# Kernel optimization log

Measured on AMD Instinct MI355X. Metric: run time of the kernel, lower is better.

Reference implementation:

```python
import jax, jax.numpy as jnp
import numpy as np

CH = 64
HEADS = 4
HD = CH // HEADS          # 16
BLOCK = 8
HALO = 1
NEIGH = BLOCK + 2 * HALO  # 10
SR = 2
HDH = HD // 2             # 8


def conv1x1(x, w, b=None):
    y = jnp.einsum('oc,bchw->bohw', w, x)
    return y if b is None else y + b[None, :, None, None]


def dw3x3(x, w, pad_mode):
    # depthwise 3x3 conv, padding=1 with given pad mode
    xp = jnp.pad(x, ((0, 0), (0, 0), (1, 1), (1, 1)), mode=pad_mode)
    return jax.lax.conv_general_dilated(
        xp, w, (1, 1), 'VALID',
        dimension_numbers=('NCHW', 'OIHW', 'NCHW'),
        feature_group_count=x.shape[1])


def maxpool2(x):
    return jax.lax.reduce_window(x, -jnp.inf, jax.lax.max, (1, 1, 2, 2), (1, 1, 2, 2), 'VALID')


def l2norm(x):
    return x / jnp.maximum(jnp.linalg.norm(x, axis=-1, keepdims=True), 1e-12)


def sorted_channel_indices(q):
    # correlation-based channel ordering (computed under no_grad in torch)
    B, C = q.shape[0], q.shape[1]
    f = jax.lax.stop_gradient(q.reshape(B, C, -1))
    cen = f - f.mean(axis=2, keepdims=True)
    cov = jnp.einsum('bcn,bdn->bcd', cen, cen)
    std = jnp.sqrt(jnp.diagonal(cov, axis1=1, axis2=2) + 1e-8)
    denom = jnp.maximum(std[:, :, None] * std[:, None, :], 1e-8)
    sim = (cov / denom).mean(axis=2)
    return jnp.argsort(-sim, axis=1)  # descending


def up_bilinear_ac(x, s):
    # bilinear upsample, align_corners=True (torch convention)
    def lerp_axis(t, axis):
        n_in = t.shape[axis]
        n_out = n_in * s
        c = jnp.arange(n_out, dtype=t.dtype) * ((n_in - 1.0) / (n_out - 1.0))
        lo = jnp.clip(jnp.floor(c).astype(jnp.int32), 0, n_in - 2)
        w = c - lo.astype(t.dtype)
        shape = [1] * t.ndim
        shape[axis] = n_out
        w = w.reshape(shape)
        return jnp.take(t, lo, axis=axis) * (1 - w) + jnp.take(t, lo + 1, axis=axis) * w
    return lerp_axis(lerp_axis(x, 2), 3)


def _forward(x, qkv_w, lce_w, gate_w, gate_b, temp, rel_h_emb, rel_w_emb,
             down_w, down_b, up_w, up_b, gating_w, gating_b, proj_w, lp_w, lp_b):
    x_in = maxpool2(x)                         # sr=2 sampler
    B, C, H, W = x_in.shape                    # H,W divisible by BLOCK -> no pad branch
    hb, wb = H // BLOCK, W // BLOCK
    BL = B * hb * wb

    qkv = dw3x3(conv1x1(x_in, qkv_w), lce_w, 'constant')   # qkv_conv + lce
    q, k, v = jnp.split(qkv, 3, axis=1)

    idx = sorted_channel_indices(q)
    gidx = idx[:, :, None, None]
    q_s = jnp.take_along_axis(q, gidx, axis=1)
    k_s = jnp.take_along_axis(k, gidx, axis=1)
    v_s = jnp.take_along_axis(v, gidx, axis=1)

    # gating: grouped 1x1 conv, one [HD,HD] matmul per head
    qh = q_s.reshape(B, HEADS, HD, H, W)
    gate_score = jnp.einsum('goc,bgcxy->bgoxy', gate_w, qh) + gate_b[None, :, :, None, None]

    # query blocks: [BL, heads, block*block, hd]
    qi = qh.reshape(B, HEADS, HD, hb, BLOCK, wb, BLOCK)
    qi = qi.transpose(0, 3, 5, 1, 4, 6, 2).reshape(BL, HEADS, BLOCK * BLOCK, HD)

    def halo_patches(t):
        # F.unfold(kernel=NEIGH, stride=BLOCK, padding=HALO), zero pad
        tp = jnp.pad(t, ((0, 0), (0, 0), (HALO, HALO), (HALO, HALO)))
        ridx = jnp.arange(hb)[:, None] * BLOCK + jnp.arange(NEIGH)[None, :]
        cidx = jnp.arange(wb)[:, None] * BLOCK + jnp.arange(NEIGH)[None, :]
        p = tp[:, :, ridx, :][..., cidx]       # [B, C, hb, NEIGH, wb, NEIGH]
        p = p.reshape(B, HEADS, HD, hb, NEIGH, wb, NEIGH).transpose(0, 3, 5, 1, 4, 6, 2)
        return p.reshape(BL, HEADS, NEIGH, NEIGH, HD)

    ks = halo_patches(k_s)
    vi = halo_patches(v_s).reshape(BL, HEADS, NEIGH * NEIGH, HD)

    # relative positional embeddings on split key channels
    kh = ks[..., :HDH] + rel_h_emb             # [BL,heads,NEIGH,NEIGH,HDH]
    kw = ks[..., HDH:] + rel_w_emb
    ki = jnp.concatenate([kh, kw], axis=-1).reshape(BL, HEADS, NEIGH * NEIGH, HD)

    logits = jnp.einsum('bhqc,bhkc->bhqk', l2norm(qi), l2norm(ki)) * jnp.exp(temp)
    attn = jax.nn.softmax(logits, axis=-1)
    out_i = jnp.einsum('bhqk,bhkc->bhqc', attn, vi)

    out = out_i.reshape(B, hb, wb, HEADS, BLOCK, BLOCK, HD)
    out = out.transpose(0, 3, 6, 1, 4, 2, 5).reshape(B, HEADS, HD, H, W)
    out = (out * jax.nn.sigmoid(gate_score)).reshape(B, C, H, W)

    cache = q_s + k_s
    inv = jnp.argsort(idx, axis=1)[:, :, None, None]
    out = jnp.take_along_axis(out, inv, axis=1)
    cache = jnp.take_along_axis(cache, inv, axis=1)

    # Intra_CacheModulation
    mixed = out + cache
    g = jax.nn.gelu(conv1x1(mixed, gating_w, gating_b), approximate=False) * mixed
    out = out + conv1x1(conv1x1(g, down_w, down_b), up_w, up_b)

    out = conv1x1(out, proj_w)
    # LocalProp: depthwise 3x3 reflect-pad conv + bilinear x2 (align_corners=True)
    out = dw3x3(out, lp_w, 'reflect') + lp_b[None, :, None, None]
    out = up_bilinear_ac(out, SR)
    # final F.interpolate to input size is identity here (shapes already match)
    return out


def setup_inputs() -> dict:
    key = jax.random.key(0)
    ks = jax.random.split(key, 12)
    B, H, W = 4, 256, 256
    p = lambda k, shape, s=0.02: jax.random.normal(k, shape, jnp.float32) * s
    return {
        'x': jax.random.normal(ks[0], (B, CH, H, W), jnp.float32),
        'qkv_w': p(ks[1], (3 * CH, CH), 0.05),
        'lce_w': p(ks[2], (3 * CH, 1, 3, 3), 0.1),
        'gate_w': p(ks[3], (HEADS, HD, HD), 0.1),
        'gate_b': jnp.ones((HEADS, HD), jnp.float32),
        'temp': jnp.zeros((1, HEADS, 1, 1), jnp.float32),
        'rel_h_emb': p(ks[4], (1, HEADS, NEIGH, 1, HDH)),
        'rel_w_emb': p(ks[5], (1, HEADS, 1, NEIGH, HD - HDH)),
        'down_w': p(ks[6], (CH // 2, CH), 0.05),
        'down_b': jnp.zeros((CH // 2,), jnp.float32),
        'up_w': p(ks[7], (CH, CH // 2), 0.05),
        'up_b': jnp.zeros((CH,), jnp.float32),
        'gating_w': p(ks[8], (CH, CH), 0.05),
        'gating_b': jnp.zeros((CH,), jnp.float32),
        'proj_w': p(ks[9], (CH, CH), 0.05),
        'lp_w': p(ks[10], (CH, 1, 3, 3), 0.1),
        'lp_b': jnp.zeros((CH,), jnp.float32),
    }


def reference(x, qkv_w, lce_w, gate_w, gate_b, temp, rel_h_emb, rel_w_emb,
              down_w, down_b, up_w, up_b, gating_w, gating_b, proj_w, lp_w, lp_b):
    return _forward(x, qkv_w, lce_w, gate_w, gate_b, temp, rel_h_emb, rel_w_emb,
                    down_w, down_b, up_w, up_b, gating_w, gating_b, proj_w, lp_w, lp_b)
```

## Files before the change

### kernel.cpp

```cpp
#include <hip/hip_runtime.h>
#include <math.h>

#define HWP 16384

static const size_t PRE_OFF  = 0;
static const size_t QKV_OFF  = 12582912;
static const size_t WT_OFF   = QKV_OFF;
static const size_t COVP_OFF = 0;
static const size_t MEAN_OFF = 2097152;
static const size_t COVS_OFF = 2097408;
static const size_t KHAT_OFF = 0;
static const size_t VPK_OFF  = 6553600;
static const size_t OUT3_OFF = 0;
static const size_t IDX_OFF  = 12570112;
static const size_t INV_OFF  = 12570368;
static const size_t GT2_OFF  = 12570624;
static const size_t DT2_OFF  = 12574720;
static const size_t UT2_OFF  = 12576768;
static const size_t PT2_OFF  = 12578816;

__global__ __launch_bounds__(256) void k_prep_wt(
    const float* __restrict__ qkv_w, float* __restrict__ wT) {
  int i = blockIdx.x * 256 + threadIdx.x;
  int o = i >> 6, c = i & 63;
  wT[c * 192 + o] = qkv_w[i];
}

__global__ __launch_bounds__(256) void k_prep2(
    const float* __restrict__ gating_w, const float* __restrict__ down_w,
    const float* __restrict__ up_w, const float* __restrict__ proj_w,
    float* __restrict__ gT, float* __restrict__ dT,
    float* __restrict__ uT, float* __restrict__ pT) {
  int t = blockIdx.x * 256 + threadIdx.x;
  if (t < 4096) {
    int o = t >> 6, d = t & 63;
    gT[d * 64 + o] = gating_w[t];
    pT[d * 64 + o] = proj_w[t];
  }
  if (t < 2048) {
    int o = t >> 6, d = t & 63;
    dT[d * 32 + o] = down_w[t];
    int o2 = t >> 5, d2 = t & 31;
    uT[d2 * 64 + o2] = up_w[t];
  }
}

__global__ __launch_bounds__(256) void k_pool_conv(
    const float* __restrict__ x, const float* __restrict__ wT,
    float* __restrict__ pre) {
  int b = blockIdx.x >> 8;
  int pix0 = (blockIdx.x & 255) * 64;
  __shared__ float xt[64 * 64];
  int t = threadIdx.x;
  for (int i = 0; i < 16; ++i) {
    int f = i * 256 + t;
    int c = f >> 6, p = f & 63;
    int pix = pix0 + p;
    int y = pix >> 7, xx = pix & 127;
    const float* src = x + ((size_t)(b * 64 + c) * 65536) + (2 * y) * 256 + 2 * xx;
    float2 v01 = *(const float2*)src;
    float2 v23 = *(const float2*)(src + 256);
    xt[c * 64 + p] = fmaxf(fmaxf(v01.x, v01.y), fmaxf(v23.x, v23.y));
  }
  __syncthreads();
  int p = t & 63;
  int obase = __builtin_amdgcn_readfirstlane((t >> 6) * 48);
  const float* wbase = wT + obase;
  float acc[48];
#pragma unroll
  for (int j = 0; j < 48; ++j) acc[j] = 0.f;
  for (int c = 0; c < 64; ++c) {
    float xv = xt[c * 64 + p];
    const float* wc = wbase + c * 192;
#pragma unroll
    for (int j = 0; j < 48; ++j) acc[j] = fmaf(wc[j], xv, acc[j]);
  }
  float* dst = pre + ((size_t)b * 192 + obase) * HWP + pix0 + p;
#pragma unroll
  for (int j = 0; j < 48; ++j) dst[(size_t)j * HWP] = acc[j];
}

__global__ __launch_bounds__(256) void k_dw3x3_zero(
    const float* __restrict__ pre, const float* __restrict__ lce_w,
    float* __restrict__ qkv) {
  int gid = blockIdx.x * 256 + threadIdx.x;
  int c4 = gid & 31;
  int y  = (gid >> 5) & 127;
  int bc = gid >> 12;
  int ch = bc % 192;
  int x0 = c4 * 4;
  const float* base = pre + (size_t)bc * HWP;
  const float* w = lce_w + ch * 9;
  const float4 z4 = make_float4(0.f, 0.f, 0.f, 0.f);
  bool ym = y > 0, yp = y < 127;
  bool xl = x0 > 0, xr = x0 < 124;
  const float* rowm = base + (y - 1) * 128;
  const float* rowc = base + y * 128;
  const float* rowp = base + (y + 1) * 128;
  float4 vm = ym ? *(const float4*)(rowm + x0) : z4;
  float  lm = (ym && xl) ? rowm[x0 - 1] : 0.f;
  float  rm = (ym && xr) ? rowm[x0 + 4] : 0.f;
  float4 vc = *(const float4*)(rowc + x0);
  float  lc = xl ? rowc[x0 - 1] : 0.f;
  float  rc = xr ? rowc[x0 + 4] : 0.f;
  float4 vp = yp ? *(const float4*)(rowp + x0) : z4;
  float  lp = (yp && xl) ? rowp[x0 - 1] : 0.f;
  float  rp = (yp && xr) ? rowp[x0 + 4] : 0.f;
  float w0 = w[0], w1 = w[1], w2 = w[2], w3 = w[3], w4 = w[4],
        w5 = w[5], w6 = w[6], w7 = w[7], w8 = w[8];
  float4 o;
  o.x = fmaf(w8, vp.y, fmaf(w7, vp.x, fmaf(w6, lp,
        fmaf(w5, vc.y, fmaf(w4, vc.x, fmaf(w3, lc,
        fmaf(w2, vm.y, fmaf(w1, vm.x, fmaf(w0, lm, 0.f)))))))));
  o.y = fmaf(w8, vp.z, fmaf(w7, vp.y, fmaf(w6, vp.x,
        fmaf(w5, vc.z, fmaf(w4, vc.y, fmaf(w3, vc.x,
        fmaf(w2, vm.z, fmaf(w1, vm.y, fmaf(w0, vm.x, 0.f)))))))));
  o.z = fmaf(w8, vp.w, fmaf(w7, vp.z, fmaf(w6, vp.y,
        fmaf(w5, vc.w, fmaf(w4, vc.z, fmaf(w3, vc.y,
        fmaf(w2, vm.w, fmaf(w1, vm.z, fmaf(w0, vm.y, 0.f)))))))));
  o.w = fmaf(w8, rp,   fmaf(w7, vp.w, fmaf(w6, vp.z,
        fmaf(w5, rc,   fmaf(w4, vc.w, fmaf(w3, vc.z,
        fmaf(w2, rm,   fmaf(w1, vm.w, fmaf(w0, vm.z, 0.f)))))))));
  *(float4*)(qkv + (size_t)bc * HWP + y * 128 + x0) = o;
}

__global__ __launch_bounds__(256) void k_mean(
    const float* __restrict__ qkv, float* __restrict__ mean) {
  int bc = blockIdx.x;
  int b = bc >> 6, c = bc & 63;
  const float* src = qkv + ((size_t)b * 192 + c) * HWP;
  float s = 0.f;
  for (int i = threadIdx.x; i < HWP; i += 256) s += src[i];
  __shared__ float red[4];
  for (int off = 32; off > 0; off >>= 1) s += __shfl_down(s, off);
  int t = threadIdx.x;
  if ((t & 63) == 0) red[t >> 6] = s;
  __syncthreads();
  if (t == 0) mean[bc] = (red[0] + red[1] + red[2] + red[3]) * (1.f / 16384.f);
}

__global__ __launch_bounds__(256) void k_covpart(
    const float* __restrict__ qkv, const float* __restrict__ mean,
    float* __restrict__ covp) {
  int blk = blockIdx.x;
  int b = blk >> 7, chunk = blk & 127;
  int e0 = chunk * 128;
  __shared__ float qc[64 * 129];
  int t = threadIdx.x;
  for (int i = 0; i < 32; ++i) {
    int f = i * 256 + t;
    int c = f >> 7, e = f & 127;
    qc[c * 129 + e] = qkv[((size_t)b * 192 + c) * HWP + e0 + e] - mean[b * 64 + c];
  }
  __syncthreads();
  int d = t & 63;
  int crow = t >> 6;
  float acc[16];
#pragma unroll
  for (int i = 0; i < 16; ++i) acc[i] = 0.f;
  for (int e = 0; e < 128; ++e) {
    float qd = qc[d * 129 + e];
#pragma unroll
    for (int i = 0; i < 16; ++i) {
      int c = crow + 4 * i;
      acc[i] = fmaf(qc[c * 129 + e], qd, acc[i]);
    }
  }
  float* dst = covp + (size_t)blk * 4096;
#pragma unroll
  for (int i = 0; i < 16; ++i) {
    int c = crow + 4 * i;
    dst[c * 64 + d] = acc[i];
  }
}

__global__ __launch_bounds__(256) void k_covred(
    const float* __restrict__ covp, float* __restrict__ covs) {
  int blk = blockIdx.x;
  int b = blk >> 4;
  int pp = (blk & 15) * 256 + threadIdx.x;
  const float* src = covp + (size_t)b * 524288 + pp;
  float s = 0.f;
  for (int ch = 0; ch < 128; ++ch) s += src[ch * 4096];
  covs[b * 4096 + pp] = s;
}

__global__ __launch_bounds__(256) void k_simsort(
    const float* __restrict__ covs_g, int* __restrict__ idx, int* __restrict__ inv) {
  int b = blockIdx.x;
  __shared__ float covs[4096];
  __shared__ float stds[64];
  __shared__ float sims[64];
  int t = threadIdx.x;
  for (int i = 0; i < 16; ++i) covs[i * 256 + t] = covs_g[b * 4096 + i * 256 + t];
  __syncthreads();
  if (t < 64) stds[t] = sqrtf(covs[t * 64 + t] + 1e-8f);
  __syncthreads();
  if (t < 64) {
    float s = 0.f;
    float sc = stds[t];
    for (int d2 = 0; d2 < 64; ++d2) {
      float denom = fmaxf(sc * stds[d2], 1e-8f);
      s += covs[d2 * 64 + t] / denom;
    }
    sims[t] = s * (1.f / 64.f);
  }
  __syncthreads();
  if (t < 64) {
    float sv = sims[t];
    int r = 0;
    for (int d2 = 0; d2 < 64; ++d2) {
      float o = sims[d2];
      if (o > sv || (o == sv && d2 < t)) r++;
    }
    idx[b * 64 + r] = t;
    inv[b * 64 + t] = r;
  }
}

__global__ __launch_bounds__(64) void k_stage(
    const float* __restrict__ qkv, const int* __restrict__ idx,
    const float* __restrict__ rel_h, const float* __restrict__ rel_w,
    float* __restrict__ khat, float* __restrict__ vpk) {
  int bi = blockIdx.x;
  int head = bi & 3;
  int wj = (bi >> 2) & 15;
  int hi = (bi >> 6) & 15;
  int b = bi >> 10;
  int t = threadIdx.x;
  const size_t bb = (size_t)b * 192 * HWP;
  int chg[16];
#pragma unroll
  for (int ch = 0; ch < 16; ++ch) chg[ch] = idx[b * 64 + head * 16 + ch];
  for (int i = 0; i < 2; ++i) {
    int pos = i * 64 + t;
    if (pos < 100) {
      int py = pos / 10, px = pos - py * 10;
      int ky = hi * 8 + py - 1, kx = wj * 8 + px - 1;
      bool ok = (ky >= 0) && (ky < 128) && (kx >= 0) && (kx < 128);
      int sp = ky * 128 + kx;
      float kv[16];
      float s = 0.f;
#pragma unroll
      for (int ch = 0; ch < 16; ++ch) {
        float k = ok ? qkv[bb + (size_t)(64 + chg[ch]) * HWP + sp] : 0.f;
        k += (ch < 8) ? rel_h[(head * 10 + py) * 8 + ch]
                      : rel_w[(head * 10 + px) * 8 + (ch - 8)];
        kv[ch] = k;
        s += k * k;
      }
      float rn = 1.f / fmaxf(sqrtf(s), 1e-12f);
      float* kd = khat + ((size_t)bi * 100 + pos) * 16;
#pragma unroll
      for (int ch = 0; ch < 16; ++ch) kd[ch] = kv[ch] * rn;
    }
  }
  int qy = hi * 8 + (t >> 3), qx = wj * 8 + (t & 7);
  int spq = qy * 128 + qx;
  float* vd = vpk + ((size_t)(b * 4 + head) * 16384 + spq) * 16;
#pragma unroll
  for (int ch = 0; ch < 16; ++ch)
    vd[ch] = qkv[bb + (size_t)(128 + chg[ch]) * HWP + spq];
}

__global__ __launch_bounds__(128) void k_attn(
    const float* __restrict__ qkv, const int* __restrict__ idx,
    const float* __restrict__ khat, const float* __restrict__ vpk,
    const float* __restrict__ gate_w, const float* __restrict__ gate_b,
    const float* __restrict__ temp, float* __restrict__ attn_out) {
  int bi = blockIdx.x;
  int head = bi & 3;
  int wj = (bi >> 2) & 15;
  int hi = (bi >> 6) & 15;
  int b = bi >> 10;
  int tt = threadIdx.x;
  int t = tt & 63;
  int w = __builtin_amdgcn_readfirstlane(tt >> 6);
  __shared__ __align__(16) float smem[3200];
  float* kr = smem;
  float* vr = smem + 1600;
  const size_t bb = (size_t)b * 192 * HWP;
  const float* kg = khat + (size_t)bi * 1600;
  for (int f = tt; f < 400; f += 128)
    ((float4*)kr)[f] = ((const float4*)kg)[f];
  const float* vb = vpk + (size_t)(b * 4 + head) * (16384 * 16);
  for (int f = tt; f < 400; f += 128) {
    int pos = f >> 2, comp = f & 3;
    int py = pos / 10, px = pos - py * 10;
    int ky = hi * 8 + py - 1, kx = wj * 8 + px - 1;
    bool ok = (ky >= 0) && (ky < 128) && (kx >= 0) && (kx < 128);
    float4 v = make_float4(0.f, 0.f, 0.f, 0.f);
    if (ok) v = ((const float4*)(vb + (size_t)(ky * 128 + kx) * 16))[comp];
    ((float4*)vr)[f] = v;
  }
  int chg[16];
#pragma unroll
  for (int ch = 0; ch < 16; ++ch) chg[ch] = idx[b * 64 + head * 16 + ch];
  int qy = hi * 8 + (t >> 3), qx = wj * 8 + (t & 7);
  float q[16];
  float qs = 0.f;
#pragma unroll
  for (int ch = 0; ch < 16; ++ch) {
    q[ch] = qkv[bb + (size_t)chg[ch] * HWP + qy * 128 + qx];
    qs += q[ch] * q[ch];
  }
  float T = expf(temp[head]);
  float qnT = T / fmaxf(sqrtf(qs), 1e-12f);
  __syncthreads();
  float out[16];
#pragma unroll
  for (int ch = 0; ch < 16; ++ch) out[ch] = 0.f;
  float wsum = 0.f;
  for (int pyl = 0; pyl < 5; ++pyl) {
    int py = w * 5 + pyl;
    const float* kp0 = kr + py * 160;
    const float* vp0 = vr + py * 160;
    for (int px = 0; px < 10; ++px) {
      const float* kp = kp0 + px * 16;
      const float* vp = vp0 + px * 16;
      float d0 = 0.f, d1 = 0.f, d2 = 0.f, d3 = 0.f;
#pragma unroll
      for (int ch = 0; ch < 4; ++ch) {
        d0 = fmaf(q[ch], kp[ch], d0);
        d1 = fmaf(q[ch + 4], kp[ch + 4], d1);
        d2 = fmaf(q[ch + 8], kp[ch + 8], d2);
        d3 = fmaf(q[ch + 12], kp[ch + 12], d3);
      }
      float dacc = (d0 + d1) + (d2 + d3);
      float e = __expf(fmaf(dacc, qnT, -T));
      wsum += e;
#pragma unroll
      for (int ch = 0; ch < 16; ++ch)
        out[ch] = fmaf(e, vp[ch], out[ch]);
    }
  }
  __syncthreads();
  float* po = smem;
  float* pwp = smem + 2048;
  pwp[w * 64 + t] = wsum;
#pragma unroll
  for (int ch = 0; ch < 16; ++ch) po[(w * 16 + ch) * 64 + t] = out[ch];
  __syncthreads();
  float winv = 1.f / (pwp[t] + pwp[64 + t]);
  int ob = w * 8;
#pragma unroll
  for (int i = 0; i < 8; ++i) {
    int o = ob + i;
    float oc = po[o * 64 + t] + po[(16 + o) * 64 + t];
    float gsv = gate_b[head * 16 + o];
#pragma unroll
    for (int c = 0; c < 16; ++c)
      gsv = fmaf(gate_w[head * 256 + o * 16 + c], q[c], gsv);
    float sig = 1.f / (1.f + __expf(-gsv));
    attn_out[bb + (size_t)(128 + chg[o]) * HWP + qy * 128 + qx] = oc * winv * sig;
  }
}

__global__ __launch_bounds__(256) void k_post(
    const float* __restrict__ attn, const float* __restrict__ qkv,
    const float* __restrict__ gT, const float* __restrict__ gating_b,
    const float* __restrict__ dT, const float* __restrict__ down_b,
    const float* __restrict__ uT, const float* __restrict__ up_b,
    const float* __restrict__ pT, float* __restrict__ out3) {
  __shared__ float xs[64 * 64];
  int t = threadIdx.x;
  int lane = t & 63;
  int w = t >> 6;
  int p = blockIdx.x * 64 + lane;
  int b = p >> 14;
  int pix = p & 16383;
  const float* ap = attn + ((size_t)b * 192 + 128) * HWP + pix;
  const float* qp = qkv + (size_t)b * 192 * HWP + pix;
  float* op = out3 + (size_t)b * 64 * HWP + pix;
  int ob16 = __builtin_amdgcn_readfirstlane(w * 16);
  int ob8  = __builtin_amdgcn_readfirstlane(w * 8);
#pragma unroll
  for (int i = 0; i < 16; ++i) {
    int c = ob16 + i;
    xs[c * 64 + lane] = ap[(size_t)c * HWP] + qp[(size_t)c * HWP] + qp[(size_t)(64 + c) * HWP];
  }
  __syncthreads();
  {
    float acc[16];
#pragma unroll
    for (int o = 0; o < 16; ++o) acc[o] = gating_b[ob16 + o];
    for (int d = 0; d < 64; ++d) {
      float xv = xs[d * 64 + lane];
      const float* wd = gT + d * 64 + ob16;
#pragma unroll
      for (int o = 0; o < 16; ++o) acc[o] = fmaf(wd[o], xv, acc[o]);
    }
    __syncthreads();
#pragma unroll
    for (int o = 0; o < 16; ++o) {
      float a = acc[o];
      float ge = 0.5f * a * (1.f + erff(a * 0.70710678118654752f));
      xs[(ob16 + o) * 64 + lane] = ge * xs[(ob16 + o) * 64 + lane];
    }
    __syncthreads();
  }
  {
    float acc[8];
#pragma unroll
    for (int o = 0; o < 8; ++o) acc[o] = down_b[ob8 + o];
    for (int d = 0; d < 64; ++d) {
      float xv = xs[d * 64 + lane];
      const float* wd = dT + d * 32 + ob8;
#pragma unroll
      for (int o = 0; o < 8; ++o) acc[o] = fmaf(wd[o], xv, acc[o]);
    }
    __syncthreads();
#pragma unroll
    for (int o = 0; o < 8; ++o) xs[(ob8 + o) * 64 + lane] = acc[o];
    __syncthreads();
  }
  {
    float acc[16];
#pragma unroll
    for (int o = 0; o < 16; ++o) acc[o] = up_b[ob16 + o];
    for (int d = 0; d < 32; ++d) {
      float xv = xs[d * 64 + lane];
      const float* wd = uT + d * 64 + ob16;
#pragma unroll
      for (int o = 0; o < 16; ++o) acc[o] = fmaf(wd[o], xv, acc[o]);
    }
    __syncthreads();
#pragma unroll
    for (int o = 0; o < 16; ++o)
      xs[(ob16 + o) * 64 + lane] = acc[o] + ap[(size_t)(ob16 + o) * HWP];
    __syncthreads();
  }
  {
    float acc[16];
#pragma unroll
    for (int o = 0; o < 16; ++o) acc[o] = 0.f;
    for (int d = 0; d < 64; ++d) {
      float xv = xs[d * 64 + lane];
      const float* wd = pT + d * 64 + ob16;
#pragma unroll
      for (int o = 0; o < 16; ++o) acc[o] = fmaf(wd[o], xv, acc[o]);
    }
#pragma unroll
    for (int o = 0; o < 16; ++o) op[(size_t)(ob16 + o) * HWP] = acc[o];
  }
}

__global__ __launch_bounds__(256) void k_final(
    const float* __restrict__ out3, const float* __restrict__ lp_w,
    const float* __restrict__ lp_b, float* __restrict__ out) {
  int bi = blockIdx.x;
  int rt = bi & 7;
  int bc = bi >> 3;
  int ch = bc & 63;
  int r0 = rt * 16;
  __shared__ float tin[20 * 128];
  __shared__ float tdw[18 * 128];
  int t = threadIdx.x;
  const float* src = out3 + (size_t)bc * HWP;
  for (int i = 0; i < 10; ++i) {
    int f = i * 256 + t;
    int r = f >> 7, xx = f & 127;
    int ry = r0 - 2 + r;
    ry = ry < 0 ? -ry : (ry > 127 ? 254 - ry : ry);
    tin[f] = src[ry * 128 + xx];
  }
  __syncthreads();
  float w0 = lp_w[ch * 9 + 0], w1 = lp_w[ch * 9 + 1], w2 = lp_w[ch * 9 + 2];
  float w3 = lp_w[ch * 9 + 3], w4 = lp_w[ch * 9 + 4], w5 = lp_w[ch * 9 + 5];
  float w6 = lp_w[ch * 9 + 6], w7 = lp_w[ch * 9 + 7], w8 = lp_w[ch * 9 + 8];
  float bias = lp_b[ch];
  for (int i = 0; i < 9; ++i) {
    int f = i * 256 + t;
    int r = f >> 7, xx = f & 127;
    int xm = (xx == 0) ? 1 : xx - 1;
    int xp = (xx == 127) ? 126 : xx + 1;
    const float* r0p = tin + r * 128;
    const float* r1p = r0p + 128;
    const float* r2p = r1p + 128;
    float acc = bias;
    acc = fmaf(w0, r0p[xm], acc); acc = fmaf(w1, r0p[xx], acc); acc = fmaf(w2, r0p[xp], acc);
    acc = fmaf(w3, r1p[xm], acc); acc = fmaf(w4, r1p[xx], acc); acc = fmaf(w5, r1p[xp], acc);
    acc = fmaf(w6, r2p[xm], acc); acc = fmaf(w7, r2p[xx], acc); acc = fmaf(w8, r2p[xp], acc);
    tdw[f] = acc;
  }
  __syncthreads();
  const float s = (float)(127.0 / 255.0);
  float* dst = out + (size_t)bc * 65536;
  for (int i = 0; i < 32; ++i) {
    int f = i * 256 + t;
    int vr = f >> 8, vx = f & 255;
    int v = 2 * r0 + vr;
    float cy = (float)v * s;
    int ly = (int)floorf(cy); if (ly > 126) ly = 126;
    float wy = cy - (float)ly;
    float cx = (float)vx * s;
    int lx = (int)floorf(cx); if (lx > 126) lx = 126;
    float wx = cx - (float)lx;
    int lr = ly - r0 + 1;
    float a  = tdw[lr * 128 + lx];
    float bq = tdw[lr * 128 + lx + 1];
    float c2 = tdw[(lr + 1) * 128 + lx];
    float d2 = tdw[(lr + 1) * 128 + lx + 1];
    float t0 = a  * (1.f - wy) + c2 * wy;
    float t1 = bq * (1.f - wy) + d2 * wy;
    dst[v * 256 + vx] = t0 * (1.f - wx) + t1 * wx;
  }
}

extern "C" void kernel_launch(void* const* d_in, const int* in_sizes, int n_in,
                              void* d_out, int out_size, void* d_ws, size_t ws_size,
                              hipStream_t stream) {
  (void)in_sizes; (void)n_in; (void)out_size; (void)ws_size;
  const float* x        = (const float*)d_in[0];
  const float* qkv_w    = (const float*)d_in[1];
  const float* lce_w    = (const float*)d_in[2];
  const float* gate_w   = (const float*)d_in[3];
  const float* gate_b   = (const float*)d_in[4];
  const float* temp     = (const float*)d_in[5];
  const float* rel_h    = (const float*)d_in[6];
  const float* rel_w    = (const float*)d_in[7];
  const float* down_w   = (const float*)d_in[8];
  const float* down_b   = (const float*)d_in[9];
  const float* up_w     = (const float*)d_in[10];
  const float* up_b     = (const float*)d_in[11];
  const float* gating_w = (const float*)d_in[12];
  const float* gating_b = (const float*)d_in[13];
  const float* proj_w   = (const float*)d_in[14];
  const float* lp_w     = (const float*)d_in[15];
  const float* lp_b     = (const float*)d_in[16];
  float* fws = (float*)d_ws;
  float* outp = (float*)d_out;

  float* pre  = fws + PRE_OFF;
  float* qkv  = fws + QKV_OFF;
  float* khat = fws + KHAT_OFF;
  float* vpk  = fws + VPK_OFF;
  float* out3 = fws + OUT3_OFF;
  float* covp = fws + COVP_OFF;
  float* mean = fws + MEAN_OFF;
  int* idx = (int*)(fws + IDX_OFF);
  int* inv = (int*)(fws + INV_OFF);
  float* covs = fws + COVS_OFF;
  float* wT   = fws + WT_OFF;
  float* gT   = fws + GT2_OFF;
  float* dT   = fws + DT2_OFF;
  float* uT   = fws + UT2_OFF;
  float* pT   = fws + PT2_OFF;

  k_prep_wt<<<48, 256, 0, stream>>>(qkv_w, wT);
  k_pool_conv<<<1024, 256, 0, stream>>>(x, wT, pre);
  k_dw3x3_zero<<<12288, 256, 0, stream>>>(pre, lce_w, qkv);
  k_prep2<<<16, 256, 0, stream>>>(gating_w, down_w, up_w, proj_w, gT, dT, uT, pT);
  k_mean<<<256, 256, 0, stream>>>(qkv, mean);
  k_covpart<<<512, 256, 0, stream>>>(qkv, mean, covp);
  k_covred<<<64, 256, 0, stream>>>(covp, covs);
  k_simsort<<<4, 256, 0, stream>>>(covs, idx, inv);
  k_stage<<<4096, 64, 0, stream>>>(qkv, idx, rel_h, rel_w, khat, vpk);
  k_attn<<<4096, 128, 0, stream>>>(qkv, idx, khat, vpk, gate_w, gate_b, temp, qkv);
  k_post<<<1024, 256, 0, stream>>>(qkv, qkv, gT, gating_b, dT, down_b,
                                   uT, up_b, pT, out3);
  k_final<<<2048, 256, 0, stream>>>(out3, lp_w, lp_b, outp);
  (void)inv;
}
```

Before: 399.3 us.

## Fuse key/value staging into attention kernel and write attention to separate buffer

Removes the k_stage kernel. The attention kernel now gathers the halo K values, adds the relative embeddings, L2-normalises them and loads V directly into shared memory from qkv. This drops the khat/vpk round trip through global memory and one launch. The halo K/V are now reread from qkv in channel-strided form by each block, and only 100 of 128 threads do the staging. Attention output goes to a dedicated compact buffer instead of overwriting the V region of qkv.

Result: faster. 369.7 us (-7.4%).

```diff
diff --git a/kernel.cpp b/kernel.cpp
--- a/kernel.cpp
+++ b/kernel.cpp
@@ -9,9 +9,8 @@
 static const size_t COVP_OFF = 0;
 static const size_t MEAN_OFF = 2097152;
 static const size_t COVS_OFF = 2097408;
-static const size_t KHAT_OFF = 0;
-static const size_t VPK_OFF  = 6553600;
-static const size_t OUT3_OFF = 0;
+static const size_t ATTN_OFF = 0;
+static const size_t OUT3_OFF = 4194304;
 static const size_t IDX_OFF  = 12570112;
 static const size_t INV_OFF  = 12570368;
 static const size_t GT2_OFF  = 12570624;
@@ -218,54 +217,9 @@
   }
 }
 
-__global__ __launch_bounds__(64) void k_stage(
+__global__ __launch_bounds__(128) void k_attn(
     const float* __restrict__ qkv, const int* __restrict__ idx,
     const float* __restrict__ rel_h, const float* __restrict__ rel_w,
-    float* __restrict__ khat, float* __restrict__ vpk) {
-  int bi = blockIdx.x;
-  int head = bi & 3;
-  int wj = (bi >> 2) & 15;
-  int hi = (bi >> 6) & 15;
-  int b = bi >> 10;
-  int t = threadIdx.x;
-  const size_t bb = (size_t)b * 192 * HWP;
-  int chg[16];
-#pragma unroll
-  for (int ch = 0; ch < 16; ++ch) chg[ch] = idx[b * 64 + head * 16 + ch];
-  for (int i = 0; i < 2; ++i) {
-    int pos = i * 64 + t;
-    if (pos < 100) {
-      int py = pos / 10, px = pos - py * 10;
-      int ky = hi * 8 + py - 1, kx = wj * 8 + px - 1;
-      bool ok = (ky >= 0) && (ky < 128) && (kx >= 0) && (kx < 128);
-      int sp = ky * 128 + kx;
-      float kv[16];
-      float s = 0.f;
-#pragma unroll
-      for (int ch = 0; ch < 16; ++ch) {
-        float k = ok ? qkv[bb + (size_t)(64 + chg[ch]) * HWP + sp] : 0.f;
-        k += (ch < 8) ? rel_h[(head * 10 + py) * 8 + ch]
-                      : rel_w[(head * 10 + px) * 8 + (ch - 8)];
-        kv[ch] = k;
-        s += k * k;
-      }
-      float rn = 1.f / fmaxf(sqrtf(s), 1e-12f);
-      float* kd = khat + ((size_t)bi * 100 + pos) * 16;
-#pragma unroll
-      for (int ch = 0; ch < 16; ++ch) kd[ch] = kv[ch] * rn;
-    }
-  }
-  int qy = hi * 8 + (t >> 3), qx = wj * 8 + (t & 7);
-  int spq = qy * 128 + qx;
-  float* vd = vpk + ((size_t)(b * 4 + head) * 16384 + spq) * 16;
-#pragma unroll
-  for (int ch = 0; ch < 16; ++ch)
-    vd[ch] = qkv[bb + (size_t)(128 + chg[ch]) * HWP + spq];
-}
-
-__global__ __launch_bounds__(128) void k_attn(
-    const float* __restrict__ qkv, const int* __restrict__ idx,
-    const float* __restrict__ khat, const float* __restrict__ vpk,
     const float* __restrict__ gate_w, const float* __restrict__ gate_b,
     const float* __restrict__ temp, float* __restrict__ attn_out) {
   int bi = blockIdx.x;
@@ -280,22 +234,31 @@
   float* kr = smem;
   float* vr = smem + 1600;
   const size_t bb = (size_t)b * 192 * HWP;
-  const float* kg = khat + (size_t)bi * 1600;
-  for (int f = tt; f < 400; f += 128)
-    ((float4*)kr)[f] = ((const float4*)kg)[f];
-  const float* vb = vpk + (size_t)(b * 4 + head) * (16384 * 16);
-  for (int f = tt; f < 400; f += 128) {
-    int pos = f >> 2, comp = f & 3;
-    int py = pos / 10, px = pos - py * 10;
+  int chg[16];
+#pragma unroll
+  for (int ch = 0; ch < 16; ++ch) chg[ch] = idx[b * 64 + head * 16 + ch];
+  if (tt < 100) {
+    int py = tt / 10, px = tt - py * 10;
     int ky = hi * 8 + py - 1, kx = wj * 8 + px - 1;
     bool ok = (ky >= 0) && (ky < 128) && (kx >= 0) && (kx < 128);
-    float4 v = make_float4(0.f, 0.f, 0.f, 0.f);
-    if (ok) v = ((const float4*)(vb + (size_t)(ky * 128 + kx) * 16))[comp];
-    ((float4*)vr)[f] = v;
-  }
-  int chg[16];
-#pragma unroll
-  for (int ch = 0; ch < 16; ++ch) chg[ch] = idx[b * 64 + head * 16 + ch];
+    int sp = ky * 128 + kx;
+    float kv[16];
+    float s = 0.f;
+#pragma unroll
+    for (int ch = 0; ch < 16; ++ch) {
+      float k = ok ? qkv[bb + (size_t)(64 + chg[ch]) * HWP + sp] : 0.f;
+      k += (ch < 8) ? rel_h[(head * 10 + py) * 8 + ch]
+                    : rel_w[(head * 10 + px) * 8 + (ch - 8)];
+      kv[ch] = k;
+      s += k * k;
+    }
+    float rn = 1.f / fmaxf(sqrtf(s), 1e-12f);
+#pragma unroll
+    for (int ch = 0; ch < 16; ++ch) kr[tt * 16 + ch] = kv[ch] * rn;
+#pragma unroll
+    for (int ch = 0; ch < 16; ++ch)
+      vr[tt * 16 + ch] = ok ? qkv[bb + (size_t)(128 + chg[ch]) * HWP + sp] : 0.f;
+  }
   int qy = hi * 8 + (t >> 3), qx = wj * 8 + (t & 7);
   float q[16];
   float qs = 0.f;
@@ -352,7 +315,7 @@
     for (int c = 0; c < 16; ++c)
       gsv = fmaf(gate_w[head * 256 + o * 16 + c], q[c], gsv);
     float sig = 1.f / (1.f + __expf(-gsv));
-    attn_out[bb + (size_t)(128 + chg[o]) * HWP + qy * 128 + qx] = oc * winv * sig;
+    attn_out[((size_t)b * 64 + chg[o]) * HWP + qy * 128 + qx] = oc * winv * sig;
   }
 }
 
@@ -369,7 +332,7 @@
   int p = blockIdx.x * 64 + lane;
   int b = p >> 14;
   int pix = p & 16383;
-  const float* ap = attn + ((size_t)b * 192 + 128) * HWP + pix;
+  const float* ap = attn + (size_t)b * 64 * HWP + pix;
   const float* qp = qkv + (size_t)b * 192 * HWP + pix;
   float* op = out3 + (size_t)b * 64 * HWP + pix;
   int ob16 = __builtin_amdgcn_readfirstlane(w * 16);
@@ -533,8 +496,7 @@
 
   float* pre  = fws + PRE_OFF;
   float* qkv  = fws + QKV_OFF;
-  float* khat = fws + KHAT_OFF;
-  float* vpk  = fws + VPK_OFF;
+  float* attn = fws + ATTN_OFF;
   float* out3 = fws + OUT3_OFF;
   float* covp = fws + COVP_OFF;
   float* mean = fws + MEAN_OFF;
@@ -555,9 +517,8 @@
   k_covpart<<<512, 256, 0, stream>>>(qkv, mean, covp);
   k_covred<<<64, 256, 0, stream>>>(covp, covs);
   k_simsort<<<4, 256, 0, stream>>>(covs, idx, inv);
-  k_stage<<<4096, 64, 0, stream>>>(qkv, idx, rel_h, rel_w, khat, vpk);
-  k_attn<<<4096, 128, 0, stream>>>(qkv, idx, khat, vpk, gate_w, gate_b, temp, qkv);
-  k_post<<<1024, 256, 0, stream>>>(qkv, qkv, gT, gating_b, dT, down_b,
+  k_attn<<<4096, 128, 0, stream>>>(qkv, idx, rel_h, rel_w, gate_w, gate_b, temp, attn);
+  k_post<<<1024, 256, 0, stream>>>(attn, qkv, gT, gating_b, dT, down_b,
                                    uT, up_b, pT, out3);
   k_final<<<2048, 256, 0, stream>>>(out3, lp_w, lp_b, outp);
   (void)inv;
```
